# Kernel tuning notes

Hardware: AMD Instinct MI355X
Metric: run time of the kernel (lower is better)

The kernel has to match this reference:

```python
import jax, jax.numpy as jnp
import numpy as np

EPS = 1e-4
SLOPE = 0.01
NFFT = 512
HOP = 256
CH_IN = 8
CH_H = 64
FREQ = NFFT // 2 + 1
LEN = 48000
BATCH = 2


def hann(n):
    return (0.5 - 0.5 * jnp.cos(2.0 * np.pi * jnp.arange(n) / n)).astype(jnp.float32)


def stft(x):
    # x: (B, C, L) -> (B, 2, C, F, T)  (torch.stft: center=True, reflect pad, hann window)
    pad = NFFT // 2
    xp = jnp.pad(x, ((0, 0), (0, 0), (pad, pad)), mode='reflect')
    T = 1 + x.shape[-1] // HOP
    idx = jnp.arange(T)[:, None] * HOP + jnp.arange(NFFT)[None, :]
    frames = xp[..., idx] * hann(NFFT)            # (B, C, T, NFFT)
    sp = jnp.fft.rfft(frames, axis=-1)            # (B, C, T, F)
    sp = jnp.swapaxes(sp, -1, -2)                 # (B, C, F, T)
    return jnp.stack([sp.real, sp.imag], axis=1).astype(jnp.float32)


def istft(re, im, length):
    # re, im: (B, C, F, T) -> (B, C, length) via windowed overlap-add
    sp = jnp.swapaxes(re + 1j * im, -1, -2)       # (B, C, T, F)
    win = hann(NFFT)
    frames = jnp.fft.irfft(sp, n=NFFT, axis=-1) * win
    pad = NFFT // 2
    total = length + 2 * pad
    T = frames.shape[-2]
    idx = jnp.arange(T)[:, None] * HOP + jnp.arange(NFFT)[None, :]
    out = jnp.zeros(frames.shape[:-2] + (total,), frames.dtype).at[..., idx].add(frames)
    wsum = jnp.zeros((total,), frames.dtype).at[idx].add(jnp.broadcast_to(win ** 2, (T, NFFT)))
    return (out / jnp.maximum(wsum, 1e-11))[..., pad:pad + length]


def conv2d(x, w, b, padT=0):
    y = jax.lax.conv_general_dilated(x, w, (1, 1), ((0, 0), (padT, padT)),
                                     dimension_numbers=('NCHW', 'OIHW', 'NCHW'))
    return y + b[None, :, None, None]


def cconv(x, w, b, padT=0):
    # complex conv on x: (B,2,C,F,T); w: (2,O,C,kf,kt) = [W_real, W_imag]; b: (2,O)
    r = conv2d(x[:, 0], w[0], b[0], padT) - conv2d(x[:, 1], w[1], b[1], padT)
    i = conv2d(x[:, 1], w[0], b[0], padT) + conv2d(x[:, 0], w[1], b[1], padT)
    return jnp.stack([r, i], axis=1)


def modExp(x, m=5.0):
    em = float(np.exp(m))
    return jnp.where(x > m, (x - m) * em + em, jnp.exp(jnp.minimum(x, m)))


def cExp(t):
    e = modExp(t[:, 0]) - 1.0
    return jnp.stack([e * jnp.cos(t[:, 1] - 1.0), e * jnp.sin(t[:, 1] - 1.0)], axis=1)


def snap(x):
    x = jnp.where((x >= 0) & (x < EPS), EPS, x)
    return jnp.where((x < 0) & (x > -EPS), -EPS, x)


def cLog(t):
    re = snap(t[:, 0])
    im = snap(t[:, 1])
    real = jnp.log(jnp.sqrt(im ** 2 + re ** 2 + EPS ** 2) + 1.0)
    imag = jnp.arctan(im / re)
    return jnp.stack([real, imag], axis=1)


def cMul(a, b):
    r = a[:, 0] * b[:, 0] - a[:, 1] * b[:, 1]
    i = a[:, 0] * b[:, 1] + a[:, 1] * b[:, 0]
    return jnp.stack([r, i], axis=1)


def trelu(t, tr, b):
    nr = t[:, 0] * tr[0, 0] + t[:, 1] * tr[0, 1] + b[0]
    ni = t[:, 0] * tr[1, 0] + t[:, 1] * tr[1, 1] + b[1]
    return jnp.stack([jax.nn.leaky_relu(nr, SLOPE), jax.nn.leaky_relu(ni, SLOPE)], axis=1)


def tgate(t, tr, b):
    gr = jax.nn.sigmoid(t[:, 0] * tr[0, 0] + t[:, 1] * tr[0, 1] + b[0])
    gi = jax.nn.sigmoid(t[:, 0] * tr[1, 0] + t[:, 1] * tr[1, 1] + b[1])
    return gr * gi + (1.0 - gr) * (1.0 - gi)


def perm(t):
    return jnp.transpose(t, (0, 1, 3, 2, 4))


def lrelu(x):
    return jax.nn.leaky_relu(x, SLOPE)


def forward(mix, fs_w, fs_b, fr_w, fr_b, c1r_w, c1r_b, c1i_w, c1i_b, c1_w, c1_b,
            c2r_w, c2r_b, c2i_w, c2i_b, c2_w, c2_b, a1_t, a1_b, a2_t, a2_b,
            c3r_w, c3r_b, c3i_w, c3i_b, c3_w, c3_b, c4r_w, c4r_b, c4i_w, c4i_b,
            c4_w, c4_b, a3_t, a3_b, a4_t, a4_b, f1_w, f1_b, f2_w, f2_b,
            cw_w, cw_b, fg_t, fg_b):
    ts = perm(cconv(perm(stft(mix)), fs_w, fs_b))      # (B,2,C,F,T)
    # ---- branch 1 ----
    tl = cLog(ts)
    tl = jnp.stack([conv2d(tl[:, 0], c1r_w, c1r_b), conv2d(tl[:, 1], c1r_w, c1r_b)], 1)
    tl = jnp.stack([conv2d(lrelu(tl[:, 0]), c1i_w, c1i_b), conv2d(tl[:, 1], c1i_w, c1i_b)], 1)
    tl = trelu(cExp(tl), a1_t, a1_b)
    t = cconv(tl, c1_w, c1_b)
    tl = cLog(t)
    tl = jnp.stack([conv2d(tl[:, 0], c2r_w, c2r_b, 7), conv2d(tl[:, 1], c2r_w, c2r_b, 7)], 1)[..., :-7]
    tl = jnp.stack([conv2d(lrelu(tl[:, 0]), c2i_w, c2i_b, 7), conv2d(tl[:, 1], c2i_w, c2i_b, 7)], 1)[..., :-7]
    tl = cExp(tl)
    tl1 = tl
    tc = cconv(ts, c2_w, c2_b, 7)[..., :-7]
    t = trelu(cMul(tl, tc), a2_t, a2_b)
    t = cconv(t, f1_w, f1_b)
    td1 = jnp.sum(ts - t, axis=2, keepdims=True) / ts.shape[2]
    # ---- branch 2 ----
    tl = cLog(ts)
    tl = jnp.stack([conv2d(tl[:, 0], c3r_w, c3r_b), conv2d(tl[:, 1], c3r_w, c3r_b)], 1)
    tl = jnp.stack([conv2d(lrelu(tl[:, 0]), c3i_w, c3i_b), conv2d(tl[:, 1], c3i_w, c3i_b)], 1)
    tl = trelu(cExp(tl), a3_t, a3_b)
    t = cconv(tl, c3_w, c3_b)
    tl = cLog(t)
    tl = jnp.stack([conv2d(tl[:, 0], c4r_w, c4r_b, 7), conv2d(tl[:, 1], c4r_w, c4r_b, 7)], 1)[..., :-7]
    tl = jnp.stack([conv2d(lrelu(tl[:, 0]), c4i_w, c4i_b, 7), conv2d(tl[:, 1], c4i_w, c4i_b, 7)], 1)[..., :-7]
    tl = cExp(tl)
    tc = cconv(ts, c4_w, c4_b, 7)[..., :-7]
    t = trelu(cMul(tl, tc), a4_t, a4_b)
    td2 = cconv(t, f2_w, f2_b)                         # (B,2,1,F,T)
    # ---- fuse ----
    f = cconv(jnp.concatenate([tl1, tl], axis=2), cw_w, cw_b)
    f = tgate(f, fg_t, fg_b)[:, None]                  # (B,1,1,F,T)
    td = td1 * f + td2 * (1.0 - f)
    t = perm(cconv(perm(td), fr_w, fr_b))
    return istft(t[:, 0], t[:, 1], LEN)                # (B,1,LEN)


def setup_inputs() -> dict:
    ks = iter(jax.random.split(jax.random.key(0), 64))
    def rn(shape, s=0.05):
        return s * jax.random.normal(next(ks), shape, jnp.float32)
    F, C, H = FREQ, CH_IN, CH_H
    inp = {
        'mix': jax.random.normal(next(ks), (BATCH, C, LEN), jnp.float32),
        'fs_w': rn((2, F, F, 1, 1)), 'fs_b': rn((2, F), 0.01),
        'fr_w': rn((2, F, F, 1, 1)), 'fr_b': rn((2, F), 0.01),
        'c1r_w': rn((H, C, 1, 1)), 'c1r_b': rn((H,), 0.01),
        'c1i_w': rn((H, H, 1, 1)), 'c1i_b': rn((H,), 0.01),
        'c1_w': rn((2, H, H, 1, 1)), 'c1_b': rn((2, H), 0.01),
        'c2r_w': rn((H, H, 1, 8)), 'c2r_b': rn((H,), 0.01),
        'c2i_w': rn((H, H, 1, 8)), 'c2i_b': rn((H,), 0.01),
        'c2_w': rn((2, H, C, 1, 8)), 'c2_b': rn((2, H), 0.01),
        'a1_t': rn((2, 2, H, F, 1), 0.5), 'a1_b': rn((2, H, F, 1), 0.5),
        'a2_t': rn((2, 2, H, F, 1), 0.5), 'a2_b': rn((2, H, F, 1), 0.5),
        'c3r_w': rn((H, C, 1, 1)), 'c3r_b': rn((H,), 0.01),
        'c3i_w': rn((H, H, 1, 1)), 'c3i_b': rn((H,), 0.01),
        'c3_w': rn((2, H, H, 1, 1)), 'c3_b': rn((2, H), 0.01),
        'c4r_w': rn((H, H, 1, 8)), 'c4r_b': rn((H,), 0.01),
        'c4i_w': rn((H, H, 1, 8)), 'c4i_b': rn((H,), 0.01),
        'c4_w': rn((2, H, C, 1, 8)), 'c4_b': rn((2, H), 0.01),
        'a3_t': rn((2, 2, H, F, 1), 0.5), 'a3_b': rn((2, H, F, 1), 0.5),
        'a4_t': rn((2, 2, H, F, 1), 0.5), 'a4_b': rn((2, H, F, 1), 0.5),
        'f1_w': rn((2, C, H, 1, 1)), 'f1_b': rn((2, C), 0.01),
        'f2_w': rn((2, 1, H, 1, 1)), 'f2_b': rn((2, 1), 0.01),
        'cw_w': rn((2, 1, 2 * H, 1, 1)), 'cw_b': rn((2, 1), 0.01),
        'fg_t': rn((2, 2, 1, F, 1), 0.5), 'fg_b': rn((2, 1, F, 1), 0.5),
    }
    return inp


def reference(mix, fs_w, fs_b, fr_w, fr_b, c1r_w, c1r_b, c1i_w, c1i_b, c1_w, c1_b,
              c2r_w, c2r_b, c2i_w, c2i_b, c2_w, c2_b, a1_t, a1_b, a2_t, a2_b,
              c3r_w, c3r_b, c3i_w, c3i_b, c3_w, c3_b, c4r_w, c4r_b, c4i_w, c4i_b,
              c4_w, c4_b, a3_t, a3_b, a4_t, a4_b, f1_w, f1_b, f2_w, f2_b,
              cw_w, cw_b, fg_t, fg_b):
    return forward(mix, fs_w, fs_b, fr_w, fr_b, c1r_w, c1r_b, c1i_w, c1i_b, c1_w, c1_b,
                   c2r_w, c2r_b, c2i_w, c2i_b, c2_w, c2_b, a1_t, a1_b, a2_t, a2_b,
                   c3r_w, c3r_b, c3i_w, c3i_b, c3_w, c3_b, c4r_w, c4r_b, c4i_w, c4i_b,
                   c4_w, c4_b, a3_t, a3_b, a4_t, a4_b, f1_w, f1_b, f2_w, f2_b,
                   cw_w, cw_b, fg_t, fg_b)
```

## Files before the change

### kernel.cpp

```cpp
#include <hip/hip_runtime.h>
#include <math.h>

#define DEV __device__ __forceinline__

constexpr int B_   = 2;
constexpr int C_IN = 8;
constexpr int H_   = 64;
constexpr int F_   = 257;
constexpr int T_   = 188;
constexpr int TW   = 96;
constexpr int NFFT = 512;
constexpr int HOP  = 256;
constexpr int LEN  = 48000;
constexpr int PADL = 256;
constexpr int FT   = F_ * T_;
constexpr float EPSV  = 1e-4f;
constexpr float SLOPEV = 0.01f;
constexpr float PI2 = 6.283185307179586f;

typedef __attribute__((ext_vector_type(8))) short short8;
typedef __attribute__((ext_vector_type(4))) short short4v;
typedef __attribute__((ext_vector_type(4))) float float4v;

DEV float lrelu_f(float x) { return x > 0.f ? x : SLOPEV * x; }
DEV float snap_f(float x) {
  if (x >= 0.f && x < EPSV) return EPSV;
  if (x < 0.f && x > -EPSV) return -EPSV;
  return x;
}
DEV float modexp_f(float x) {
  const float em = 148.4131591025766f;
  return x > 5.f ? (x - 5.f) * em + em : expf(x);
}
DEV void cexp_f(float tr, float ti, float& er, float& ei) {
  float e = modexp_f(tr) - 1.f;
  float s, c;
  sincosf(ti - 1.f, &s, &c);
  er = e * c; ei = e * s;
}
DEV float sigmoid_f(float x) { return 1.f / (1.f + expf(-x)); }

DEV short f2bf(float x) {
  unsigned u = __float_as_uint(x);
  unsigned r = (u + 0x7fffu + ((u >> 16) & 1u)) >> 16;
  return (short)r;
}
DEV float bf2f(short h) {
  return __uint_as_float(((unsigned)(unsigned short)h) << 16);
}

__global__ void k_mixsplit(const float* __restrict__ x, short* __restrict__ hi,
                           short* __restrict__ lo) {
  int i = blockIdx.x * 256 + threadIdx.x;
  if (i >= B_ * C_IN * LEN / 4) return;
  float4v v = *(const float4v*)(x + (size_t)i * 4);
  short4v h, l;
  #pragma unroll
  for (int j = 0; j < 4; ++j) {
    h[j] = f2bf(v[j]);
    l[j] = f2bf(v[j] - bf2f(h[j]));
  }
  *(short4v*)(hi + (size_t)i * 4) = h;
  *(short4v*)(lo + (size_t)i * 4) = l;
}

__global__ __launch_bounds__(256) void k_mixdft(const float* __restrict__ W,
                                                short* __restrict__ wpk) {
  constexpr int MT = 33;
  __shared__ float wr_s[F_], wi_s[F_];
  int m = blockIdx.x;
  int k = blockIdx.y * 256 + threadIdx.x;
  int po = m >= F_;
  int fo = m - po * F_;
  if (m < 2 * F_) {
    for (int i = threadIdx.x; i < F_; i += 256) {
      wr_s[i] = W[fo * F_ + i];
      wi_s[i] = W[F_ * F_ + fo * F_ + i];
    }
  }
  __syncthreads();
  float val = 0.f;
  if (m < 2 * F_) {
    float sd, cd;
    sincosf((PI2 / NFFT) * k, &sd, &cd);
    float cs = 1.f, sn = 0.f;
    float ar = 0.f, ai = 0.f;
    for (int fi = 0; fi < F_; ++fi) {
      float wrv = wr_s[fi], wiv = wi_s[fi];
      ar += wrv * cs + wiv * sn;
      ai += wiv * cs - wrv * sn;
      float t2 = cs * cd - sn * sd;
      sn = sn * cd + cs * sd;
      cs = t2;
    }
    float win = 0.5f - 0.5f * cd;
    val = (po ? ai : ar) * win;
  }
  int mtg = m >> 4;
  int lane2 = ((k >> 3) & 3) * 16 + (m & 15);
  int s = k >> 5;
  int j = k & 7;
  short hi = f2bf(val);
  short lo = f2bf(val - bf2f(hi));
  wpk[(((0 * 16 + s) * MT + mtg) * 64 + lane2) * 8 + j] = hi;
  wpk[(((16 + s) * MT + mtg) * 64 + lane2) * 8 + j] = lo;
}

__global__ __launch_bounds__(256) void k_stftmix(
    const short* __restrict__ mhi, const short* __restrict__ mlo,
    const short* __restrict__ wpk, const float* __restrict__ bias,
    float* __restrict__ Y) {
  constexpr int PITCH = 136;
  constexpr int MT = 33;
  __shared__ short xs_hi[TW * PITCH];
  __shared__ short xs_lo[TW * PITCH];
  int mg = blockIdx.x;
  int bc = blockIdx.y;
  int b = bc >> 3, c = bc & 7;
  int t0 = blockIdx.z * TW;
  int tid = threadIdx.x;
  int lane = tid & 63;
  int wv = __builtin_amdgcn_readfirstlane(tid >> 6);
  int mh = wv >> 1;
  int tc = wv & 1;
  int q = lane >> 4;
  int n = lane & 15;
  int wbase = tc * 48;

  const short* mh_ = mhi + (size_t)(b * C_IN + c) * LEN;
  const short* ml_ = mlo + (size_t)(b * C_IN + c) * LEN;

  float4v acc[2][3];
  #pragma unroll
  for (int mt = 0; mt < 2; ++mt)
    #pragma unroll
    for (int nt = 0; nt < 3; ++nt) acc[mt][nt] = (float4v)(0.f);

  const short8* wp = (const short8*)wpk;
  for (int round = 0; round < 4; ++round) {
    if (round) __syncthreads();
    for (int i = tid; i < TW * 16; i += 256) {
      int tl = i >> 4, u = i & 15;
      int kk0 = u * 8;
      int t = t0 + tl;
      int g0 = t * HOP + round * 128 + kk0 - PADL;
      short8 h, l;
      if (t < T_ && g0 >= 0 && g0 + 7 < LEN) {
        h = *(const short8*)(mh_ + g0);
        l = *(const short8*)(ml_ + g0);
      } else {
        #pragma unroll
        for (int j = 0; j < 8; ++j) {
          short hv = 0, lv = 0;
          if (t < T_) {
            int g = g0 + j;
            if (g < 0) g = -g;
            if (g >= LEN) g = 2 * LEN - 2 - g;
            hv = mh_[g]; lv = ml_[g];
          }
          h[j] = hv; l[j] = lv;
        }
      }
      *(short8*)&xs_hi[tl * PITCH + kk0] = h;
      *(short8*)&xs_lo[tl * PITCH + kk0] = l;
    }
    __syncthreads();
    #pragma unroll
    for (int s2 = 0; s2 < 4; ++s2) {
      int s = round * 4 + s2;
      short8 Bh[3], Bl[3];
      #pragma unroll
      for (int nt = 0; nt < 3; ++nt) {
        int off = (wbase + nt * 16 + n) * PITCH + s2 * 32 + q * 8;
        Bh[nt] = *(const short8*)&xs_hi[off];
        Bl[nt] = *(const short8*)&xs_lo[off];
      }
      #pragma unroll
      for (int mt = 0; mt < 2; ++mt) {
        int mtg = mg * 4 + mh * 2 + mt;
        if (mtg >= MT) continue;
        short8 Ah = wp[((0 * 16 + s) * MT + mtg) * 64 + lane];
        short8 Al = wp[((16 + s) * MT + mtg) * 64 + lane];
        #pragma unroll
        for (int nt = 0; nt < 3; ++nt) {
          acc[mt][nt] = __builtin_amdgcn_mfma_f32_16x16x32_bf16(Ah, Bh[nt], acc[mt][nt], 0, 0, 0);
          acc[mt][nt] = __builtin_amdgcn_mfma_f32_16x16x32_bf16(Ah, Bl[nt], acc[mt][nt], 0, 0, 0);
          acc[mt][nt] = __builtin_amdgcn_mfma_f32_16x16x32_bf16(Al, Bh[nt], acc[mt][nt], 0, 0, 0);
        }
      }
    }
  }

  #pragma unroll
  for (int nt = 0; nt < 3; ++nt) {
    int t = t0 + wbase + nt * 16 + n;
    if (t >= T_) continue;
    #pragma unroll
    for (int mt = 0; mt < 2; ++mt) {
      int mtg = mg * 4 + mh * 2 + mt;
      if (mtg >= MT) continue;
      #pragma unroll
      for (int r = 0; r < 4; ++r) {
        int m = mtg * 16 + q * 4 + r;
        if (m >= 2 * F_) continue;
        int po = m >= F_;
        int fo = m - po * F_;
        float badd = po ? bias[fo] + bias[F_ + fo] : bias[fo] - bias[F_ + fo];
        Y[((size_t)((b * 2 + po) * C_IN + c)) * FT + fo * T_ + t] = acc[mt][nt][r] + badd;
      }
    }
  }
}

template<int CH>
__global__ void k_fmix(const float* __restrict__ X, const float* __restrict__ W,
                       const float* __restrict__ bias, float* __restrict__ Y) {
  int fo = blockIdx.x;
  int bc = blockIdx.y; int c = bc % CH; int b = bc / CH;
  int t = threadIdx.x;
  if (t >= T_) return;
  const float* wr = W + fo * F_;
  const float* wi = W + F_ * F_ + fo * F_;
  const float* xr = X + ((b * 2 + 0) * CH + c) * FT + t;
  const float* xi = X + ((b * 2 + 1) * CH + c) * FT + t;
  float ar = 0.f, ai = 0.f;
  for (int fi = 0; fi < F_; ++fi) {
    float wrv = wr[fi], wiv = wi[fi];
    float xrv = xr[fi * T_], xiv = xi[fi * T_];
    ar += wrv * xrv - wiv * xiv;
    ai += wrv * xiv + wiv * xrv;
  }
  float br = bias[fo], bi = bias[F_ + fo];
  Y[((b * 2 + 0) * CH + c) * FT + fo * T_ + t] = ar + br - bi;
  Y[((b * 2 + 1) * CH + c) * FT + fo * T_ + t] = ai + br + bi;
}

template<int CIN, int K>
DEV void repack_real_body(const float* __restrict__ W, short* __restrict__ wpk, int i) {
  constexpr int CC = (CIN >= 32) ? (CIN / 32) : 1;
  constexpr int NSTEP = (CIN * K + 31) / 32;
  int total = 2 * NSTEP * 4 * 64 * 8;
  if (i >= total) return;
  int j = i & 7;
  int lane = (i >> 3) & 63;
  int mt = (i >> 9) & 3;
  int s = (i >> 11) % NSTEP;
  int split = i / (NSTEP * 2048);
  int q = lane >> 4;
  int m = mt * 16 + (lane & 15);
  int tap = s / CC;
  int c = (s % CC) * 32 + q * 8 + j;
  float w = 0.f;
  if (c < CIN && tap < K) w = W[(m * CIN + c) * K + tap];
  short hi = f2bf(w);
  wpk[i] = split ? f2bf(w - bf2f(hi)) : hi;
}

template<int CIN2, int COUT2, int K>
DEV void repack_cplx_body(const float* __restrict__ W, short* __restrict__ wpk, int i) {
  constexpr int CIN = CIN2 / 2, COUT = COUT2 / 2;
  constexpr int NSTEP = CIN2 * K / 32;
  constexpr int MT = (COUT2 + 15) / 16;
  int total = 2 * NSTEP * MT * 64 * 8;
  if (i >= total) return;
  int j = i & 7;
  int lane = (i >> 3) & 63;
  int idx = i >> 9;
  int mt = idx % MT; idx /= MT;
  int s = idx % NSTEP;
  int split = idx / NSTEP;
  int q = lane >> 4;
  int m = mt * 16 + (lane & 15);
  int tap, pi, ci;
  if constexpr (CIN2 == 128) {
    tap = 0;
    int cs = s * 32 + q * 8 + j;
    int half = cs / 64, r = cs % 64;
    ci = half * 32 + r / 2;
    pi = r & 1;
  } else {
    tap = s * 2 + (q >> 1);
    int cs = (q & 1) * 8 + j;
    pi = cs / CIN;
    ci = cs % CIN;
  }
  float w = 0.f;
  if (m < COUT2) {
    int po = m / COUT, ho = m % COUT;
    float wr = W[((0 * COUT + ho) * CIN + ci) * K + tap];
    float wi = W[((1 * COUT + ho) * CIN + ci) * K + tap];
    w = (po == pi) ? wr : (po == 0 ? -wi : wi);
  }
  short hi = f2bf(w);
  wpk[i] = split ? f2bf(w - bf2f(hi)) : hi;
}

__global__ __launch_bounds__(256) void k_repack_all(
    const float* c1r_w, const float* c1i_w, const float* c2r_w, const float* c2i_w,
    const float* c3r_w, const float* c3i_w, const float* c4r_w, const float* c4i_w,
    const float* c1_w, const float* c2_w, const float* c3_w, const float* c4_w,
    const float* f1_w, const float* f2_w,
    short* o0, short* o1, short* o2, short* o3, short* o4, short* o5, short* o6,
    short* o7, short* o8, short* o9, short* o10, short* o11, short* o12, short* o13) {
  int i = blockIdx.x * 256 + threadIdx.x;
  switch (blockIdx.y) {
    case 0:  repack_real_body<C_IN, 1>(c1r_w, o0, i); break;
    case 1:  repack_real_body<H_,   1>(c1i_w, o1, i); break;
    case 2:  repack_real_body<H_,   8>(c2r_w, o2, i); break;
    case 3:  repack_real_body<H_,   8>(c2i_w, o3, i); break;
    case 4:  repack_real_body<C_IN, 1>(c3r_w, o4, i); break;
    case 5:  repack_real_body<H_,   1>(c3i_w, o5, i); break;
    case 6:  repack_real_body<H_,   8>(c4r_w, o6, i); break;
    case 7:  repack_real_body<H_,   8>(c4i_w, o7, i); break;
    case 8:  repack_cplx_body<128, 128, 1>(c1_w, o8, i); break;
    case 9:  repack_cplx_body<16,  128, 8>(c2_w, o9, i); break;
    case 10: repack_cplx_body<128, 128, 1>(c3_w, o10, i); break;
    case 11: repack_cplx_body<16,  128, 8>(c4_w, o11, i); break;
    case 12: repack_cplx_body<128, 16,  1>(f1_w, o12, i); break;
    case 13: repack_cplx_body<128, 2,   1>(f2_w, o13, i); break;
  }
}

template<int CIN, int K, int PRO>
__global__ __launch_bounds__(256) void k_conv_mfma(
    const float* __restrict__ X, const short* __restrict__ wpk,
    const float* __restrict__ bias, float* __restrict__ Y) {
  constexpr int CC = (CIN >= 32) ? (CIN / 32) : 1;
  constexpr int NSTEP = (CIN * K + 31) / 32;
  constexpr int PITCH = 72;
  constexpr int ROWS = TW + (K - 1);
  __shared__ short xs_hi[ROWS * PITCH];
  __shared__ short xs_lo[ROWS * PITCH];
  int f = blockIdx.x;
  int bp = blockIdx.y; int p = bp & 1; int b = bp >> 1;
  int t0 = blockIdx.z * TW;
  int tid = threadIdx.x;

  for (int i = tid; i < ROWS * PITCH; i += 256) { xs_hi[i] = 0; xs_lo[i] = 0; }
  __syncthreads();

  const float* Xr_ = X + (size_t)((b * 2 + 0) * CIN) * FT + f * T_;
  const float* Xi_ = X + (size_t)((b * 2 + 1) * CIN) * FT + f * T_;
  const float* Xp  = X + (size_t)((b * 2 + p) * CIN) * FT + f * T_;
  for (int i = tid; i < CIN * ROWS; i += 256) {
    int c = i / ROWS, rr = i % ROWS;
    int t = t0 + rr - (K - 1);
    if (t < 0 || t >= T_) continue;
    float v;
    if (PRO == 2) {
      float re = snap_f(Xr_[c * FT + t]);
      float im = snap_f(Xi_[c * FT + t]);
      v = (p == 0) ? logf(sqrtf(im * im + re * re + EPSV * EPSV) + 1.f)
                   : atanf(im / re);
    } else {
      v = Xp[c * FT + t];
      if (PRO == 1 && p == 0) v = lrelu_f(v);
    }
    short hi = f2bf(v);
    short lo = f2bf(v - bf2f(hi));
    xs_hi[rr * PITCH + c] = hi;
    xs_lo[rr * PITCH + c] = lo;
  }
  __syncthreads();

  int lane = tid & 63;
  int wv = __builtin_amdgcn_readfirstlane(tid >> 6);
  int mh = wv >> 1;
  int tc = wv & 1;
  int q = lane >> 4;
  int n = lane & 15;
  int wbase = tc * 48;

  float4v acc[2][3];
  #pragma unroll
  for (int mt = 0; mt < 2; ++mt)
    #pragma unroll
    for (int nt = 0; nt < 3; ++nt) acc[mt][nt] = (float4v)(0.f);

  const short8* wp = (const short8*)wpk;
  for (int s = 0; s < NSTEP; ++s) {
    int tap = s / CC;
    int c0 = (s % CC) * 32;
    short8 Bh[3], Bl[3];
    #pragma unroll
    for (int nt = 0; nt < 3; ++nt) {
      int off = (wbase + nt * 16 + n + tap) * PITCH + c0 + q * 8;
      Bh[nt] = *(const short8*)&xs_hi[off];
      Bl[nt] = *(const short8*)&xs_lo[off];
    }
    #pragma unroll
    for (int mt = 0; mt < 2; ++mt) {
      int mtg = mh * 2 + mt;
      short8 Ah = wp[((0 * NSTEP + s) * 4 + mtg) * 64 + lane];
      short8 Al = wp[((1 * NSTEP + s) * 4 + mtg) * 64 + lane];
      #pragma unroll
      for (int nt = 0; nt < 3; ++nt) {
        acc[mt][nt] = __builtin_amdgcn_mfma_f32_16x16x32_bf16(Ah, Bh[nt], acc[mt][nt], 0, 0, 0);
        acc[mt][nt] = __builtin_amdgcn_mfma_f32_16x16x32_bf16(Ah, Bl[nt], acc[mt][nt], 0, 0, 0);
        acc[mt][nt] = __builtin_amdgcn_mfma_f32_16x16x32_bf16(Al, Bh[nt], acc[mt][nt], 0, 0, 0);
      }
    }
  }

  float* Yp = Y + (size_t)((b * 2 + p) * H_) * FT + f * T_;
  #pragma unroll
  for (int nt = 0; nt < 3; ++nt) {
    int t = t0 + wbase + nt * 16 + n;
    if (t >= T_) continue;
    #pragma unroll
    for (int mt = 0; mt < 2; ++mt) {
      #pragma unroll
      for (int r = 0; r < 4; ++r) {
        int h = (mh * 2 + mt) * 16 + q * 4 + r;
        Yp[h * FT + t] = acc[mt][nt][r] + bias[h];
      }
    }
  }
}

template<int COUT2, int PRO>
__global__ __launch_bounds__(256) void k_cconv128(
    const float* __restrict__ X0, const float* __restrict__ X1,
    const short* __restrict__ wpk,
    const float* __restrict__ at, const float* __restrict__ ab,
    const float* __restrict__ bias, float* __restrict__ Y) {
  constexpr int MT = (COUT2 + 15) / 16;
  constexpr int MTW = (MT > 4) ? 4 : MT;
  constexpr int COUT = COUT2 / 2;
  constexpr int NSTEP = 4;
  constexpr int PITCH = 72;
  __shared__ short xs_hi[TW * PITCH];
  __shared__ short xs_lo[TW * PITCH];
  __shared__ float coef[6][64];
  int f = blockIdx.x;
  int b = blockIdx.y;
  int t0 = blockIdx.z * TW;
  int tid = threadIdx.x;
  int lane = tid & 63;
  int wv = __builtin_amdgcn_readfirstlane(tid >> 6);
  int mh = wv >> 1;
  int tc = wv & 1;
  int q = lane >> 4;
  int n = lane & 15;
  int wbase = tc * 48;

  if (tid < 64) {
    int h = tid;
    coef[0][h] = at[(0 * H_ + h) * F_ + f];
    coef[1][h] = at[(1 * H_ + h) * F_ + f];
    coef[2][h] = at[(2 * H_ + h) * F_ + f];
    coef[3][h] = at[(3 * H_ + h) * F_ + f];
    coef[4][h] = ab[h * F_ + f];
    coef[5][h] = ab[(H_ + h) * F_ + f];
  }
  for (int i = tid; i < TW * PITCH; i += 256) { xs_hi[i] = 0; xs_lo[i] = 0; }

  const float* b0r = X0 + (size_t)((b * 2 + 0) * H_) * FT + f * T_;
  const float* b0i = X0 + (size_t)((b * 2 + 1) * H_) * FT + f * T_;
  const float* b1r = X1 + (size_t)((b * 2 + 0) * H_) * FT + f * T_;
  const float* b1i = X1 + (size_t)((b * 2 + 1) * H_) * FT + f * T_;

  float4v acc[MTW][3];
  #pragma unroll
  for (int mt = 0; mt < MTW; ++mt)
    #pragma unroll
    for (int nt = 0; nt < 3; ++nt) acc[mt][nt] = (float4v)(0.f);

  const short8* wp = (const short8*)wpk;
  for (int half = 0; half < 2; ++half) {
    __syncthreads();
    for (int i = tid; i < 32 * TW; i += 256) {
      int hh = i / TW, tl = i % TW;
      int t = t0 + tl;
      if (t >= T_) continue;
      int h = half * 32 + hh;
      float xr = b0r[h * FT + t], xi = b0i[h * FT + t];
      float vr, vi;
      if (PRO == 1) {
        float er, ei;
        cexp_f(xr, xi, er, ei);
        vr = lrelu_f(er * coef[0][h] + ei * coef[1][h] + coef[4][h]);
        vi = lrelu_f(er * coef[2][h] + ei * coef[3][h] + coef[5][h]);
      } else {
        float yr = b1r[h * FT + t], yi = b1i[h * FT + t];
        float mr = xr * yr - xi * yi;
        float mi = xr * yi + xi * yr;
        vr = lrelu_f(mr * coef[0][h] + mi * coef[1][h] + coef[4][h]);
        vi = lrelu_f(mr * coef[2][h] + mi * coef[3][h] + coef[5][h]);
      }
      int cs0 = hh * 2, cs1 = hh * 2 + 1;
      short hr = f2bf(vr), hi2 = f2bf(vi);
      xs_hi[tl * PITCH + cs0] = hr;
      xs_lo[tl * PITCH + cs0] = f2bf(vr - bf2f(hr));
      xs_hi[tl * PITCH + cs1] = hi2;
      xs_lo[tl * PITCH + cs1] = f2bf(vi - bf2f(hi2));
    }
    __syncthreads();
    #pragma unroll
    for (int s2 = 0; s2 < 2; ++s2) {
      int s = half * 2 + s2;
      short8 Bh[3], Bl[3];
      #pragma unroll
      for (int nt = 0; nt < 3; ++nt) {
        int off = (wbase + nt * 16 + n) * PITCH + s2 * 32 + q * 8;
        Bh[nt] = *(const short8*)&xs_hi[off];
        Bl[nt] = *(const short8*)&xs_lo[off];
      }
      #pragma unroll
      for (int mt = 0; mt < MTW; ++mt) {
        int mtg = mh * 4 + mt;
        if (mtg >= MT) continue;
        short8 Ah = wp[((0 * NSTEP + s) * MT + mtg) * 64 + lane];
        short8 Al = wp[((1 * NSTEP + s) * MT + mtg) * 64 + lane];
        #pragma unroll
        for (int nt = 0; nt < 3; ++nt) {
          acc[mt][nt] = __builtin_amdgcn_mfma_f32_16x16x32_bf16(Ah, Bh[nt], acc[mt][nt], 0, 0, 0);
          acc[mt][nt] = __builtin_amdgcn_mfma_f32_16x16x32_bf16(Ah, Bl[nt], acc[mt][nt], 0, 0, 0);
          acc[mt][nt] = __builtin_amdgcn_mfma_f32_16x16x32_bf16(Al, Bh[nt], acc[mt][nt], 0, 0, 0);
        }
      }
    }
  }

  float* Yp = Y + (size_t)b * COUT2 * FT + f * T_;
  #pragma unroll
  for (int nt = 0; nt < 3; ++nt) {
    int t = t0 + wbase + nt * 16 + n;
    if (t >= T_) continue;
    #pragma unroll
    for (int mt = 0; mt < MTW; ++mt) {
      int mtg = mh * 4 + mt;
      if (mtg >= MT) continue;
      #pragma unroll
      for (int r = 0; r < 4; ++r) {
        int o2 = mtg * 16 + q * 4 + r;
        if (o2 >= COUT2) continue;
        int po = o2 / COUT, ho = o2 % COUT;
        float br = bias[ho], bi = bias[COUT + ho];
        float badd = (po == 0) ? br - bi : br + bi;
        Yp[o2 * FT + t] = acc[mt][nt][r] + badd;
      }
    }
  }
}

__global__ __launch_bounds__(256) void k_cconv16(
    const float* __restrict__ X, const short* __restrict__ wpk,
    const float* __restrict__ bias, float* __restrict__ Y) {
  constexpr int MT = 8, NSTEP = 4, PITCH = 24, ROWS = TW + 7, COUT = 64, COUT2 = 128;
  __shared__ short xs_hi[ROWS * PITCH];
  __shared__ short xs_lo[ROWS * PITCH];
  int f = blockIdx.x;
  int b = blockIdx.y;
  int t0 = blockIdx.z * TW;
  int tid = threadIdx.x;

  for (int i = tid; i < ROWS * PITCH; i += 256) { xs_hi[i] = 0; xs_lo[i] = 0; }
  __syncthreads();

  const float* Xp = X + (size_t)b * 16 * FT + f * T_;
  for (int i = tid; i < 16 * ROWS; i += 256) {
    int c = i / ROWS, rr = i % ROWS;
    int t = t0 + rr - 7;
    if (t < 0 || t >= T_) continue;
    float v = Xp[c * FT + t];
    short hi = f2bf(v);
    short lo = f2bf(v - bf2f(hi));
    xs_hi[rr * PITCH + c] = hi;
    xs_lo[rr * PITCH + c] = lo;
  }
  __syncthreads();

  int lane = tid & 63;
  int wv = __builtin_amdgcn_readfirstlane(tid >> 6);
  int mh = wv >> 1;
  int tc = wv & 1;
  int q = lane >> 4;
  int n = lane & 15;
  int wbase = tc * 48;

  float4v acc[4][3];
  #pragma unroll
  for (int mt = 0; mt < 4; ++mt)
    #pragma unroll
    for (int nt = 0; nt < 3; ++nt) acc[mt][nt] = (float4v)(0.f);

  const short8* wp = (const short8*)wpk;
  #pragma unroll
  for (int s = 0; s < NSTEP; ++s) {
    int tap = s * 2 + (q >> 1);
    int coff = (q & 1) * 8;
    short8 Bh[3], Bl[3];
    #pragma unroll
    for (int nt = 0; nt < 3; ++nt) {
      int off = (wbase + nt * 16 + n + tap) * PITCH + coff;
      Bh[nt] = *(const short8*)&xs_hi[off];
      Bl[nt] = *(const short8*)&xs_lo[off];
    }
    #pragma unroll
    for (int mt = 0; mt < 4; ++mt) {
      int mtg = mh * 4 + mt;
      short8 Ah = wp[((0 * NSTEP + s) * MT + mtg) * 64 + lane];
      short8 Al = wp[((1 * NSTEP + s) * MT + mtg) * 64 + lane];
      #pragma unroll
      for (int nt = 0; nt < 3; ++nt) {
        acc[mt][nt] = __builtin_amdgcn_mfma_f32_16x16x32_bf16(Ah, Bh[nt], acc[mt][nt], 0, 0, 0);
        acc[mt][nt] = __builtin_amdgcn_mfma_f32_16x16x32_bf16(Ah, Bl[nt], acc[mt][nt], 0, 0, 0);
        acc[mt][nt] = __builtin_amdgcn_mfma_f32_16x16x32_bf16(Al, Bh[nt], acc[mt][nt], 0, 0, 0);
      }
    }
  }

  float* Yp = Y + (size_t)b * COUT2 * FT + f * T_;
  #pragma unroll
  for (int nt = 0; nt < 3; ++nt) {
    int t = t0 + wbase + nt * 16 + n;
    if (t >= T_) continue;
    #pragma unroll
    for (int mt = 0; mt < 4; ++mt) {
      #pragma unroll
      for (int r = 0; r < 4; ++r) {
        int o2 = (mh * 4 + mt) * 16 + q * 4 + r;
        int po = o2 / COUT, ho = o2 % COUT;
        float br = bias[ho], bi = bias[COUT + ho];
        float badd = (po == 0) ? br - bi : br + bi;
        Yp[o2 * FT + t] = acc[mt][nt][r] + badd;
      }
    }
  }
}

__global__ void k_cexp(const float* __restrict__ X, float* __restrict__ Y) {
  int i = blockIdx.x * blockDim.x + threadIdx.x;
  if (i >= B_ * H_ * FT) return;
  int b = i / (H_ * FT);
  int r = i % (H_ * FT);
  int i0 = (b * 2) * H_ * FT + r;
  int i1 = i0 + H_ * FT;
  float er, ei;
  cexp_f(X[i0], X[i1], er, ei);
  Y[i0] = er;
  Y[i1] = ei;
}

__global__ void k_td1(const float* __restrict__ ts, const float* __restrict__ t8,
                      float* __restrict__ td1) {
  int i = blockIdx.x * blockDim.x + threadIdx.x;
  if (i >= B_ * 2 * FT) return;
  int bp = i / FT; int r = i % FT;
  const float* a = ts + bp * C_IN * FT + r;
  const float* c2 = t8 + bp * C_IN * FT + r;
  float acc = 0.f;
  #pragma unroll
  for (int c = 0; c < C_IN; ++c) acc += a[c * FT] - c2[c * FT];
  td1[i] = acc * (1.f / C_IN);
}

__global__ void k_fuse(const float* __restrict__ tl1, const float* __restrict__ tl2,
                       const float* __restrict__ td1, const float* __restrict__ td2,
                       const float* __restrict__ cw, const float* __restrict__ cwb,
                       const float* __restrict__ fgt, const float* __restrict__ fgb,
                       float* __restrict__ td) {
  int i = blockIdx.x * blockDim.x + threadIdx.x;
  if (i >= B_ * FT) return;
  int b = i / FT; int r = i % FT; int f = r / T_;
  const float* x1r = tl1 + (b * 2) * H_ * FT + r;
  const float* x1i = x1r + H_ * FT;
  const float* x2r = tl2 + (b * 2) * H_ * FT + r;
  const float* x2i = x2r + H_ * FT;
  float fr = 0.f, fi = 0.f;
  for (int c = 0; c < H_; ++c) {
    float w1r = cw[c], w2r = cw[H_ + c], w1i = cw[2 * H_ + c], w2i = cw[3 * H_ + c];
    float a1r = x1r[c * FT], a1i = x1i[c * FT];
    float a2r = x2r[c * FT], a2i = x2i[c * FT];
    fr += w1r * a1r - w1i * a1i + w2r * a2r - w2i * a2i;
    fi += w1r * a1i + w1i * a1r + w2r * a2i + w2i * a2r;
  }
  fr += cwb[0] - cwb[1];
  fi += cwb[0] + cwb[1];
  float t00 = fgt[f], t01 = fgt[F_ + f], t10 = fgt[2 * F_ + f], t11 = fgt[3 * F_ + f];
  float gr = sigmoid_f(fr * t00 + fi * t01 + fgb[f]);
  float gi = sigmoid_f(fr * t10 + fi * t11 + fgb[F_ + f]);
  float gg = gr * gi + (1.f - gr) * (1.f - gi);
  int i0 = (b * 2) * FT + r, i1 = i0 + FT;
  td[i0] = td1[i0] * gg + td2[i0] * (1.f - gg);
  td[i1] = td1[i1] * gg + td2[i1] * (1.f - gg);
}

__global__ __launch_bounds__(320) void k_iframes(const float* __restrict__ sp,
                                                 float* __restrict__ frames) {
  __shared__ float Xr[F_], Xi[F_];
  int blk = blockIdx.x;
  int t = blk % T_;
  int b = blk / T_;
  int tid = threadIdx.x;
  for (int i = tid; i < F_; i += 320) {
    Xr[i] = sp[(b * 2 + 0) * FT + i * T_ + t];
    Xi[i] = sp[(b * 2 + 1) * FT + i * T_ + t];
  }
  __syncthreads();
  int n = tid;
  if (n <= 256) {
    float sd, cd;
    sincosf((PI2 / NFFT) * n, &sd, &cd);
    float cs = cd, sn = sd;
    float ac = 0.f, as = 0.f;
    for (int f = 1; f < 256; ++f) {
      ac += Xr[f] * cs;
      as += Xi[f] * sn;
      float t2 = cs * cd - sn * sd;
      sn = sn * cd + cs * sd;
      cs = t2;
    }
    float base = Xr[0] + Xr[256] * (1.f - 2.f * (n & 1));
    float win = 0.5f - 0.5f * cd;
    float scale = win * (1.f / NFFT);
    float* fr = frames + (size_t)(b * T_ + t) * NFFT;
    fr[n] = (base + 2.f * ac - 2.f * as) * scale;
    if (n >= 1 && n <= 255)
      fr[NFFT - n] = (base + 2.f * ac + 2.f * as) * scale;
  }
}

__global__ void k_ola(const float* __restrict__ frames, float* __restrict__ out) {
  int i = blockIdx.x * blockDim.x + threadIdx.x;
  if (i >= B_ * LEN) return;
  int b = i / LEN; int j = i % LEN;
  int p = j + PADL;
  int t0 = p / HOP; int n0 = p - t0 * HOP;
  float acc = 0.f, wsum = 0.f;
  if (t0 < T_) {
    acc += frames[(b * T_ + t0) * NFFT + n0];
    float w = 0.5f - 0.5f * cosf((PI2 / NFFT) * n0);
    wsum += w * w;
  }
  int t1 = t0 - 1, n1 = n0 + HOP;
  if (t1 >= 0 && t1 < T_) {
    acc += frames[(b * T_ + t1) * NFFT + n1];
    float w = 0.5f - 0.5f * cosf((PI2 / NFFT) * n1);
    wsum += w * w;
  }
  out[i] = acc / fmaxf(wsum, 1e-11f);
}

extern "C" void kernel_launch(void* const* d_in, const int* in_sizes, int n_in,
                              void* d_out, int out_size, void* d_ws, size_t ws_size,
                              hipStream_t stream) {
  const float* mix   = (const float*)d_in[0];
  const float* fs_w  = (const float*)d_in[1];
  const float* fs_b  = (const float*)d_in[2];
  const float* fr_w  = (const float*)d_in[3];
  const float* fr_b  = (const float*)d_in[4];
  const float* c1r_w = (const float*)d_in[5];
  const float* c1r_b = (const float*)d_in[6];
  const float* c1i_w = (const float*)d_in[7];
  const float* c1i_b = (const float*)d_in[8];
  const float* c1_w  = (const float*)d_in[9];
  const float* c1_b  = (const float*)d_in[10];
  const float* c2r_w = (const float*)d_in[11];
  const float* c2r_b = (const float*)d_in[12];
  const float* c2i_w = (const float*)d_in[13];
  const float* c2i_b = (const float*)d_in[14];
  const float* c2_w  = (const float*)d_in[15];
  const float* c2_b  = (const float*)d_in[16];
  const float* a1_t  = (const float*)d_in[17];
  const float* a1_b  = (const float*)d_in[18];
  const float* a2_t  = (const float*)d_in[19];
  const float* a2_b  = (const float*)d_in[20];
  const float* c3r_w = (const float*)d_in[21];
  const float* c3r_b = (const float*)d_in[22];
  const float* c3i_w = (const float*)d_in[23];
  const float* c3i_b = (const float*)d_in[24];
  const float* c3_w  = (const float*)d_in[25];
  const float* c3_b  = (const float*)d_in[26];
  const float* c4r_w = (const float*)d_in[27];
  const float* c4r_b = (const float*)d_in[28];
  const float* c4i_w = (const float*)d_in[29];
  const float* c4i_b = (const float*)d_in[30];
  const float* c4_w  = (const float*)d_in[31];
  const float* c4_b  = (const float*)d_in[32];
  const float* a3_t  = (const float*)d_in[33];
  const float* a3_b  = (const float*)d_in[34];
  const float* a4_t  = (const float*)d_in[35];
  const float* a4_b  = (const float*)d_in[36];
  const float* f1_w  = (const float*)d_in[37];
  const float* f1_b  = (const float*)d_in[38];
  const float* f2_w  = (const float*)d_in[39];
  const float* f2_b  = (const float*)d_in[40];
  const float* cw_w  = (const float*)d_in[41];
  const float* cw_b  = (const float*)d_in[42];
  const float* fg_t  = (const float*)d_in[43];
  const float* fg_b  = (const float*)d_in[44];

  const size_t S8 = (size_t)B_ * 2 * C_IN * FT;
  const size_t SH = (size_t)B_ * 2 * H_ * FT;
  const size_t S1 = (size_t)B_ * 2 * FT;
  float* ws  = (float*)d_ws;
  float* ts0 = ws;
  float* ts  = ts0 + S8;
  float* A   = ts + S8;
  float* Bb  = A + SH;
  float* Cc  = Bb + SH;
  float* td1 = Cc + SH;
  float* td2 = td1 + S1;
  float* tdf = td2 + S1;
  float* tdr = tdf + S1;
  float* s8  = ts0;
  float* frames = ts0;

  short* wtail = (short*)(tdr + S1);
  constexpr int SZ_C8K1   = 2 * 1  * 4 * 64 * 8;
  constexpr int SZ_C64K1  = 2 * 2  * 4 * 64 * 8;
  constexpr int SZ_C64K8  = 2 * 16 * 4 * 64 * 8;
  constexpr int SZ_CC128  = 2 * 4  * 8 * 64 * 8;
  constexpr int SZ_CF     = 2 * 4  * 1 * 64 * 8;
  constexpr int SZ_SM     = 2 * 16 * 33 * 64 * 8;
  short* w_c1r = wtail;
  short* w_c1i = w_c1r + SZ_C8K1;
  short* w_c2r = w_c1i + SZ_C64K1;
  short* w_c2i = w_c2r + SZ_C64K8;
  short* w_c3r = w_c2i + SZ_C64K8;
  short* w_c3i = w_c3r + SZ_C8K1;
  short* w_c4r = w_c3i + SZ_C64K1;
  short* w_c4i = w_c4r + SZ_C64K8;
  short* w_cc1 = w_c4i + SZ_C64K8;
  short* w_cc2 = w_cc1 + SZ_CC128;
  short* w_cc3 = w_cc2 + SZ_CC128;
  short* w_cc4 = w_cc3 + SZ_CC128;
  short* w_cf1 = w_cc4 + SZ_CC128;
  short* w_cf2 = w_cf1 + SZ_CF;
  short* w_sm  = w_cf2 + SZ_CF;
  short* mhi   = w_sm + SZ_SM;
  short* mlo   = mhi + (size_t)B_ * C_IN * LEN;

  const int nH = B_ * H_ * FT;
  const int nP = B_ * FT;
  const dim3 rgrid(F_, B_ * 2, 2);
  const dim3 cgrid(F_, B_, 2);

  k_repack_all<<<dim3(256, 14), 256, 0, stream>>>(
      c1r_w, c1i_w, c2r_w, c2i_w, c3r_w, c3i_w, c4r_w, c4i_w,
      c1_w, c2_w, c3_w, c4_w, f1_w, f2_w,
      w_c1r, w_c1i, w_c2r, w_c2i, w_c3r, w_c3i, w_c4r, w_c4i,
      w_cc1, w_cc2, w_cc3, w_cc4, w_cf1, w_cf2);

  k_mixsplit<<<(B_ * C_IN * LEN / 4 + 255) / 256, 256, 0, stream>>>(mix, mhi, mlo);
  k_mixdft<<<dim3(528, 2), 256, 0, stream>>>(fs_w, w_sm);
  k_stftmix<<<dim3(9, 16, 2), 256, 0, stream>>>(mhi, mlo, w_sm, fs_b, ts);

  k_conv_mfma<C_IN, 1, 2><<<rgrid, 256, 0, stream>>>(ts, w_c1r, c1r_b, A);
  k_conv_mfma<H_, 1, 1><<<rgrid, 256, 0, stream>>>(A, w_c1i, c1i_b, Bb);
  k_cconv128<128, 1><<<cgrid, 256, 0, stream>>>(Bb, Bb, w_cc1, a1_t, a1_b, c1_b, A);
  k_conv_mfma<H_, 8, 2><<<rgrid, 256, 0, stream>>>(A, w_c2r, c2r_b, Bb);
  k_conv_mfma<H_, 8, 1><<<rgrid, 256, 0, stream>>>(Bb, w_c2i, c2i_b, A);
  k_cexp<<<(nH + 255) / 256, 256, 0, stream>>>(A, Bb);
  k_cconv16<<<cgrid, 256, 0, stream>>>(ts, w_cc2, c2_b, A);
  k_cconv128<16, 2><<<cgrid, 256, 0, stream>>>(Bb, A, w_cf1, a2_t, a2_b, f1_b, s8);
  k_td1<<<(B_ * 2 * FT + 255) / 256, 256, 0, stream>>>(ts, s8, td1);

  k_conv_mfma<C_IN, 1, 2><<<rgrid, 256, 0, stream>>>(ts, w_c3r, c3r_b, A);
  k_conv_mfma<H_, 1, 1><<<rgrid, 256, 0, stream>>>(A, w_c3i, c3i_b, Cc);
  k_cconv128<128, 1><<<cgrid, 256, 0, stream>>>(Cc, Cc, w_cc3, a3_t, a3_b, c3_b, A);
  k_conv_mfma<H_, 8, 2><<<rgrid, 256, 0, stream>>>(A, w_c4r, c4r_b, Cc);
  k_conv_mfma<H_, 8, 1><<<rgrid, 256, 0, stream>>>(Cc, w_c4i, c4i_b, A);
  k_cexp<<<(nH + 255) / 256, 256, 0, stream>>>(A, Cc);
  k_cconv16<<<cgrid, 256, 0, stream>>>(ts, w_cc4, c4_b, A);
  k_cconv128<2, 2><<<cgrid, 256, 0, stream>>>(Cc, A, w_cf2, a4_t, a4_b, f2_b, td2);

  k_fuse<<<(nP + 255) / 256, 256, 0, stream>>>(Bb, Cc, td1, td2, cw_w, cw_b, fg_t, fg_b, tdf);
  k_fmix<1><<<dim3(F_, B_), 192, 0, stream>>>(tdf, fr_w, fr_b, tdr);
  k_iframes<<<B_ * T_, 320, 0, stream>>>(tdr, frames);
  k_ola<<<(B_ * LEN + 255) / 256, 256, 0, stream>>>(frames, (float*)d_out);
}
```

Measured before the change: 864.4 us.

## Fuse two time-kernel-8 conv stages and complex exp into one kernel

Replaces the pair of k_conv_mfma launches for the 8-tap time convolutions plus the separate k_cexp pass with a single k_chain8 kernel per branch. The new kernel does the log/atan prologue, the first conv, keeps its output (with a halo) in LDS as split bf16, runs the second conv from LDS, and applies cexp before writing. This removes two full-size intermediate round trips through global memory and two launches. In exchange it recomputes halo columns on smaller 48-wide time tiles and uses a large LDS footprint, which may limit occupancy.

```diff
diff --git a/kernel.cpp b/kernel.cpp
--- a/kernel.cpp
+++ b/kernel.cpp
@@ -418,6 +418,171 @@
   }
 }
 
+constexpr int TW2 = 48;
+__global__ __launch_bounds__(256) void k_chain8(
+    const float* __restrict__ X, const short* __restrict__ wpk1,
+    const float* __restrict__ b1, const short* __restrict__ wpk2,
+    const float* __restrict__ b2, float* __restrict__ Y) {
+  constexpr int CPITCH = 72;
+  constexpr int XROWS = 72;
+  __shared__ __align__(16) short lds[4 * XROWS * CPITCH];
+  short* xh0 = lds;
+  short* xl0 = xh0 + XROWS * CPITCH;
+  short* xh1 = xl0 + XROWS * CPITCH;
+  short* xl1 = xh1 + XROWS * CPITCH;
+  int f = blockIdx.x;
+  int b = blockIdx.y;
+  int t0 = blockIdx.z * TW2;
+  int tid = threadIdx.x;
+  int lane = tid & 63;
+  int wv = __builtin_amdgcn_readfirstlane(tid >> 6);
+  int mh = wv >> 1;
+  int p = wv & 1;
+  int q = lane >> 4;
+  int n = lane & 15;
+
+  const float* Xr = X + (size_t)((b * 2 + 0) * H_) * FT + f * T_;
+  const float* Xi = X + (size_t)((b * 2 + 1) * H_) * FT + f * T_;
+
+  {
+    int cb = tid >> 6, xb = tid & 63;
+    for (int c = cb; c < H_; c += 4) {
+      const float* xr = Xr + (size_t)c * FT;
+      const float* xi = Xi + (size_t)c * FT;
+      #pragma unroll
+      for (int xo = 0; xo < XROWS; xo += 64) {
+        int x = xb + xo;
+        if (x >= XROWS) continue;
+        int t = t0 + x - 23;
+        float lg = 0.f, at = 0.f;
+        if (t >= 0 && t < T_) {
+          float re = snap_f(xr[t]);
+          float im = snap_f(xi[t]);
+          lg = logf(sqrtf(im * im + re * re + EPSV * EPSV) + 1.f);
+          at = atanf(im / re);
+        }
+        short h0 = f2bf(lg);
+        short h1 = f2bf(at);
+        xh0[x * CPITCH + c] = h0;
+        xl0[x * CPITCH + c] = f2bf(lg - bf2f(h0));
+        xh1[x * CPITCH + c] = h1;
+        xl1[x * CPITCH + c] = f2bf(at - bf2f(h1));
+      }
+    }
+  }
+  __syncthreads();
+
+  const short* bhx = p ? xh1 : xh0;
+  const short* blx = p ? xl1 : xl0;
+  const short8* wp1 = (const short8*)wpk1;
+  float4v a1[2][4];
+  #pragma unroll
+  for (int mt = 0; mt < 2; ++mt)
+    #pragma unroll
+    for (int nt = 0; nt < 4; ++nt) a1[mt][nt] = (float4v)(0.f);
+  for (int s = 0; s < 16; ++s) {
+    int tap = s >> 1;
+    int c0 = (s & 1) * 32;
+    short8 Bh[4], Bl[4];
+    #pragma unroll
+    for (int nt = 0; nt < 4; ++nt) {
+      int off = (nt * 16 + n + tap) * CPITCH + c0 + q * 8;
+      Bh[nt] = *(const short8*)&bhx[off];
+      Bl[nt] = *(const short8*)&blx[off];
+    }
+    #pragma unroll
+    for (int mt = 0; mt < 2; ++mt) {
+      int mtg = mh * 2 + mt;
+      short8 Ah = wp1[(s * 4 + mtg) * 64 + lane];
+      short8 Al = wp1[((16 + s) * 4 + mtg) * 64 + lane];
+      #pragma unroll
+      for (int nt = 0; nt < 4; ++nt) {
+        a1[mt][nt] = __builtin_amdgcn_mfma_f32_16x16x32_bf16(Ah, Bh[nt], a1[mt][nt], 0, 0, 0);
+        a1[mt][nt] = __builtin_amdgcn_mfma_f32_16x16x32_bf16(Ah, Bl[nt], a1[mt][nt], 0, 0, 0);
+        a1[mt][nt] = __builtin_amdgcn_mfma_f32_16x16x32_bf16(Al, Bh[nt], a1[mt][nt], 0, 0, 0);
+      }
+    }
+  }
+  __syncthreads();
+
+  short* zh = lds + (p * 2) * (64 * CPITCH);
+  short* zl = zh + 64 * CPITCH;
+  #pragma unroll
+  for (int nt = 0; nt < 4; ++nt) {
+    int z = nt * 16 + n;
+    int t = t0 - 16 + z;
+    bool ok = (t >= 0 && t < T_);
+    #pragma unroll
+    for (int mt = 0; mt < 2; ++mt)
+      #pragma unroll
+      for (int r = 0; r < 4; ++r) {
+        int h = (mh * 2 + mt) * 16 + q * 4 + r;
+        float v = ok ? (a1[mt][nt][r] + b1[h]) : 0.f;
+        if (p == 0) v = lrelu_f(v);
+        short hh = f2bf(v);
+        zh[z * CPITCH + h] = hh;
+        zl[z * CPITCH + h] = f2bf(v - bf2f(hh));
+      }
+  }
+  __syncthreads();
+
+  const short8* wp2 = (const short8*)wpk2;
+  float4v a2[2][3];
+  #pragma unroll
+  for (int mt = 0; mt < 2; ++mt)
+    #pragma unroll
+    for (int nt = 0; nt < 3; ++nt) a2[mt][nt] = (float4v)(0.f);
+  for (int s = 0; s < 16; ++s) {
+    int tap = s >> 1;
+    int c0 = (s & 1) * 32;
+    short8 Bh[3], Bl[3];
+    #pragma unroll
+    for (int nt = 0; nt < 3; ++nt) {
+      int off = (nt * 16 + n + tap + 9) * CPITCH + c0 + q * 8;
+      Bh[nt] = *(const short8*)&zh[off];
+      Bl[nt] = *(const short8*)&zl[off];
+    }
+    #pragma unroll
+    for (int mt = 0; mt < 2; ++mt) {
+      int mtg = mh * 2 + mt;
+      short8 Ah = wp2[(s * 4 + mtg) * 64 + lane];
+      short8 Al = wp2[((16 + s) * 4 + mtg) * 64 + lane];
+      #pragma unroll
+      for (int nt = 0; nt < 3; ++nt) {
+        a2[mt][nt] = __builtin_amdgcn_mfma_f32_16x16x32_bf16(Ah, Bh[nt], a2[mt][nt], 0, 0, 0);
+        a2[mt][nt] = __builtin_amdgcn_mfma_f32_16x16x32_bf16(Ah, Bl[nt], a2[mt][nt], 0, 0, 0);
+        a2[mt][nt] = __builtin_amdgcn_mfma_f32_16x16x32_bf16(Al, Bh[nt], a2[mt][nt], 0, 0, 0);
+      }
+    }
+  }
+  __syncthreads();
+
+  float* zf = (float*)lds;
+  #pragma unroll
+  for (int nt = 0; nt < 3; ++nt) {
+    int o = nt * 16 + n;
+    #pragma unroll
+    for (int mt = 0; mt < 2; ++mt)
+      #pragma unroll
+      for (int r = 0; r < 4; ++r) {
+        int h = (mh * 2 + mt) * 16 + q * 4 + r;
+        zf[(p * H_ + h) * 50 + o] = a2[mt][nt][r] + b2[h];
+      }
+  }
+  __syncthreads();
+  float* Yr = Y + (size_t)((b * 2 + 0) * H_) * FT + f * T_;
+  float* Yi = Y + (size_t)((b * 2 + 1) * H_) * FT + f * T_;
+  for (int i = tid; i < H_ * TW2; i += 256) {
+    int h = i / TW2, o = i % TW2;
+    int t = t0 + o;
+    if (t >= T_) continue;
+    float er, ei;
+    cexp_f(zf[h * 50 + o], zf[(H_ + h) * 50 + o], er, ei);
+    Yr[(size_t)h * FT + t] = er;
+    Yi[(size_t)h * FT + t] = ei;
+  }
+}
+
 template<int COUT2, int PRO>
 __global__ __launch_bounds__(256) void k_cconv128(
     const float* __restrict__ X0, const float* __restrict__ X1,
@@ -628,19 +793,6 @@
       }
     }
   }
-}
-
-__global__ void k_cexp(const float* __restrict__ X, float* __restrict__ Y) {
-  int i = blockIdx.x * blockDim.x + threadIdx.x;
-  if (i >= B_ * H_ * FT) return;
-  int b = i / (H_ * FT);
-  int r = i % (H_ * FT);
-  int i0 = (b * 2) * H_ * FT + r;
-  int i1 = i0 + H_ * FT;
-  float er, ei;
-  cexp_f(X[i0], X[i1], er, ei);
-  Y[i0] = er;
-  Y[i1] = ei;
 }
 
 __global__ void k_td1(const float* __restrict__ ts, const float* __restrict__ t8,
@@ -833,10 +985,10 @@
   short* mhi   = w_sm + SZ_SM;
   short* mlo   = mhi + (size_t)B_ * C_IN * LEN;
 
-  const int nH = B_ * H_ * FT;
   const int nP = B_ * FT;
   const dim3 rgrid(F_, B_ * 2, 2);
   const dim3 cgrid(F_, B_, 2);
+  const dim3 hgrid(F_, B_, 4);
 
   k_repack_all<<<dim3(256, 14), 256, 0, stream>>>(
       c1r_w, c1i_w, c2r_w, c2i_w, c3r_w, c3i_w, c4r_w, c4i_w,
@@ -851,9 +1003,7 @@
   k_conv_mfma<C_IN, 1, 2><<<rgrid, 256, 0, stream>>>(ts, w_c1r, c1r_b, A);
   k_conv_mfma<H_, 1, 1><<<rgrid, 256, 0, stream>>>(A, w_c1i, c1i_b, Bb);
   k_cconv128<128, 1><<<cgrid, 256, 0, stream>>>(Bb, Bb, w_cc1, a1_t, a1_b, c1_b, A);
-  k_conv_mfma<H_, 8, 2><<<rgrid, 256, 0, stream>>>(A, w_c2r, c2r_b, Bb);
-  k_conv_mfma<H_, 8, 1><<<rgrid, 256, 0, stream>>>(Bb, w_c2i, c2i_b, A);
-  k_cexp<<<(nH + 255) / 256, 256, 0, stream>>>(A, Bb);
+  k_chain8<<<hgrid, 256, 0, stream>>>(A, w_c2r, c2r_b, w_c2i, c2i_b, Bb);
   k_cconv16<<<cgrid, 256, 0, stream>>>(ts, w_cc2, c2_b, A);
   k_cconv128<16, 2><<<cgrid, 256, 0, stream>>>(Bb, A, w_cf1, a2_t, a2_b, f1_b, s8);
   k_td1<<<(B_ * 2 * FT + 255) / 256, 256, 0, stream>>>(ts, s8, td1);
@@ -861,9 +1011,7 @@
   k_conv_mfma<C_IN, 1, 2><<<rgrid, 256, 0, stream>>>(ts, w_c3r, c3r_b, A);
   k_conv_mfma<H_, 1, 1><<<rgrid, 256, 0, stream>>>(A, w_c3i, c3i_b, Cc);
   k_cconv128<128, 1><<<cgrid, 256, 0, stream>>>(Cc, Cc, w_cc3, a3_t, a3_b, c3_b, A);
-  k_conv_mfma<H_, 8, 2><<<rgrid, 256, 0, stream>>>(A, w_c4r, c4r_b, Cc);
-  k_conv_mfma<H_, 8, 1><<<rgrid, 256, 0, stream>>>(Cc, w_c4i, c4i_b, A);
-  k_cexp<<<(nH + 255) / 256, 256, 0, stream>>>(A, Cc);
+  k_chain8<<<hgrid, 256, 0, stream>>>(A, w_c4r, c4r_b, w_c4i, c4i_b, Cc);
   k_cconv16<<<cgrid, 256, 0, stream>>>(ts, w_cc4, c4_b, A);
   k_cconv128<2, 2><<<cgrid, 256, 0, stream>>>(Cc, A, w_cf2, a4_t, a4_b, f2_b, td2);
 
```

After: 906.7 us. 4.9% more time.
